# Performance work log

Measured on AMD Instinct MI355X. Metric: run time of the kernel, lower is better.

The kernel has to match this reference:

```python
import jax, jax.numpy as jnp
import numpy as np

N_NODES = 100000
N_EDGES = 1600000
IN_C, HID_C, OUT_C = 128, 64, 32


def setup_inputs() -> dict:
    key = jax.random.key(0)
    k1, k2, k3, k4 = jax.random.split(key, 4)
    x = jax.random.normal(k1, (N_NODES, IN_C), dtype=jnp.float32)
    edge_index = jax.random.randint(k2, (2, N_EDGES), 0, N_NODES, dtype=jnp.int64)
    # glorot-style init for GCN linear weights
    W1 = jax.random.normal(k3, (IN_C, HID_C), dtype=jnp.float32) * (2.0 / (IN_C + HID_C)) ** 0.5
    b1 = jnp.zeros((HID_C,), dtype=jnp.float32)
    W2 = jax.random.normal(k4, (HID_C, OUT_C), dtype=jnp.float32) * (2.0 / (HID_C + OUT_C)) ** 0.5
    b2 = jnp.zeros((OUT_C,), dtype=jnp.float32)
    return {"x": x, "edge_index": edge_index, "W1": W1, "b1": b1, "W2": W2, "b2": b2}


def _gcn_conv(h, row, col, norm, n, b):
    # gather transformed source features, scale by symmetric norm, scatter-add to targets
    msg = h[row] * norm[:, None]            # [E+N, C]
    return jax.ops.segment_sum(msg, col, num_segments=n) + b


def reference(x, edge_index, W1, b1, W2, b2):
    n = x.shape[0]
    loops = jnp.arange(n, dtype=edge_index.dtype)
    row = jnp.concatenate([edge_index[0], loops])   # sources (with self-loops)
    col = jnp.concatenate([edge_index[1], loops])   # targets
    deg = jax.ops.segment_sum(jnp.ones_like(col, dtype=x.dtype), col, num_segments=n)
    dinv = jnp.where(deg > 0, jax.lax.rsqrt(deg), 0.0)
    norm = dinv[row] * dinv[col]                    # D^{-1/2} A_hat D^{-1/2}
    h = jax.nn.relu(_gcn_conv(x @ W1, row, col, norm, n, b1))
    out = _gcn_conv(h @ W2, row, col, norm, n, b2)
    return out
```

## Files before the change

### kernel.cpp

```cpp
#include <hip/hip_runtime.h>

#define IN_C 128
#define HID_C 64
#define OUT_C 32
#define NBLK 512
#define NBUCK 512
#define CAP 5120

typedef unsigned int uint;
typedef unsigned short ushort;
typedef __attribute__((ext_vector_type(8))) short bf16x8;
typedef __attribute__((ext_vector_type(4))) float f32x4;

__device__ __forceinline__ uint bf16pair(float a, float b) {
  uint ua = __float_as_uint(a), ub = __float_as_uint(b);
  ua = (ua + 0x7FFFu + ((ua >> 16) & 1u)) >> 16;
  ub = (ub + 0x7FFFu + ((ub >> 16) & 1u)) >> 16;
  return ua | (ub << 16);
}

__device__ __forceinline__ uint bf16one(float a) {
  uint u = __float_as_uint(a);
  return (u + 0x7FFFu + ((u >> 16) & 1u)) >> 16;
}

__device__ __forceinline__ void acc8(float* acc, uint4 q) {
  acc[0] += __uint_as_float(q.x << 16);
  acc[1] += __uint_as_float(q.x & 0xFFFF0000u);
  acc[2] += __uint_as_float(q.y << 16);
  acc[3] += __uint_as_float(q.y & 0xFFFF0000u);
  acc[4] += __uint_as_float(q.z << 16);
  acc[5] += __uint_as_float(q.z & 0xFFFF0000u);
  acc[6] += __uint_as_float(q.w << 16);
  acc[7] += __uint_as_float(q.w & 0xFFFF0000u);
}


__global__ void __launch_bounds__(256) scatter_reserve_kernel(
    const int* __restrict__ row, const int* __restrict__ col,
    int* __restrict__ gcur, int* __restrict__ ebuf, int e, int epb) {
  __shared__ int hist[NBUCK];
  __shared__ int cur[NBUCK];
  int t = threadIdx.x, b = blockIdx.x;
  for (int i = t; i < NBUCK; i += 256) hist[i] = 0;
  __syncthreads();
  int s = b * epb, en = min(e, s + epb);
  for (int i = s + t; i < en; i += 256) atomicAdd(&hist[col[i] >> 8], 1);
  __syncthreads();
  for (int i = t; i < NBUCK; i += 256) {
    int h = hist[i];
    int base = h ? atomicAdd(&gcur[i], h) : 0;
    cur[i] = CAP * i + base;
  }
  __syncthreads();
  for (int i = s + t; i < en; i += 256) {
    int c = col[i], r = row[i];
    int bk = c >> 8;
    int p = atomicAdd(&cur[bk], 1);
    if (p < CAP * bk + CAP) ebuf[p] = r | ((c & 255) << 17);
  }
}

__global__ void __launch_bounds__(256) csr_kernel(const int* __restrict__ ebuf,
                                                  const int* __restrict__ gcur,
                                                  int* __restrict__ offS, int* __restrict__ offE,
                                                  int* __restrict__ srt, float* __restrict__ dinv,
                                                  int n) {
  __shared__ int cnt[256];
  __shared__ int base[256];
  int t = threadIdx.x, b = blockIdx.x;
  int es = b * CAP;
  int ec = min(gcur[b], CAP);
  cnt[t] = 0;
  __syncthreads();
  for (int i = t; i < ec; i += 256) atomicAdd(&cnt[(ebuf[es + i] >> 17) & 255], 1);
  __syncthreads();
  int v = cnt[t];
  base[t] = v;
  __syncthreads();
  for (int d = 1; d < 256; d <<= 1) {
    int a = (t >= d) ? base[t - d] : 0;
    __syncthreads();
    base[t] += a;
    __syncthreads();
  }
  int gstart = es + base[t] - v;
  int node = b * 256 + t;
  if (node < n) {
    offS[node] = gstart;
    offE[node] = gstart + v;
    dinv[node] = rsqrtf((float)(v + 1));
  }
  base[t] = gstart;
  __syncthreads();
  for (int i = t; i < ec; i += 256) {
    int pv = ebuf[es + i];
    int pos = atomicAdd(&base[(pv >> 17) & 255], 1);
    srt[pos] = pv & 0x1FFFF;
  }
}


__global__ void __launch_bounds__(256) prep_w_kernel(const float* __restrict__ W1,
                                                     const float* __restrict__ W2,
                                                     ushort* __restrict__ w1t_hi,
                                                     ushort* __restrict__ w1t_lo,
                                                     ushort* __restrict__ w2t_hi,
                                                     ushort* __restrict__ w2t_lo) {
  int t = threadIdx.x;
  for (int i = t; i < HID_C * IN_C; i += 256) {
    int c = i >> 7, k = i & 127;
    float v = W1[k * HID_C + c];
    uint h = bf16one(v);
    float lo = v - __uint_as_float(h << 16);
    w1t_hi[i] = (ushort)h;
    w1t_lo[i] = (ushort)bf16one(lo);
  }
  for (int i = t; i < OUT_C * HID_C; i += 256) {
    int c = i >> 6, k = i & 63;
    float v = W2[k * OUT_C + c];
    uint h = bf16one(v);
    float lo = v - __uint_as_float(h << 16);
    w2t_hi[i] = (ushort)h;
    w2t_lo[i] = (ushort)bf16one(lo);
  }
}

#define APAD 136
__global__ void __launch_bounds__(256) gemm1_mfma_kernel(
    const float* __restrict__ x, const ushort* __restrict__ w1t_hi,
    const ushort* __restrict__ w1t_lo, const float* __restrict__ dinv,
    ushort* __restrict__ xw1q, int n, int planeN) {
  __shared__ ushort xs_hi[64 * APAD];
  __shared__ ushort xs_lo[64 * APAD];
  __shared__ float dinv_s[64];
  int t = threadIdx.x;
  int row0 = blockIdx.x * 64;
  if (t < 64) {
    int rr = row0 + t;
    dinv_s[t] = rr < n ? dinv[rr] : 0.f;
  }
  for (int task = t; task < 64 * 16; task += 256) {
    int r = task >> 4, kc = task & 15;
    int grow = row0 + r;
    uint4 hq = {0u, 0u, 0u, 0u}, lq = {0u, 0u, 0u, 0u};
    if (grow < n) {
      const float* xp = x + (size_t)grow * IN_C + kc * 8;
      float4 v0 = *(const float4*)xp;
      float4 v1 = *(const float4*)(xp + 4);
      float vv[8] = {v0.x, v0.y, v0.z, v0.w, v1.x, v1.y, v1.z, v1.w};
      uint hu[8];
      float lf[8];
#pragma unroll
      for (int i = 0; i < 8; ++i) {
        hu[i] = bf16one(vv[i]);
        lf[i] = vv[i] - __uint_as_float(hu[i] << 16);
      }
      hq = make_uint4(hu[0] | (hu[1] << 16), hu[2] | (hu[3] << 16),
                      hu[4] | (hu[5] << 16), hu[6] | (hu[7] << 16));
      lq = make_uint4(bf16pair(lf[0], lf[1]), bf16pair(lf[2], lf[3]),
                      bf16pair(lf[4], lf[5]), bf16pair(lf[6], lf[7]));
    }
    *(uint4*)(xs_hi + r * APAD + kc * 8) = hq;
    *(uint4*)(xs_lo + r * APAD + kc * 8) = lq;
  }
  __syncthreads();
  int wv = t >> 6, lane = t & 63, m = lane & 15, q = lane >> 4;
  f32x4 acc[4];
#pragma unroll
  for (int ct = 0; ct < 4; ++ct) acc[ct] = (f32x4){0.f, 0.f, 0.f, 0.f};
  const ushort* ah_p = xs_hi + (wv * 16 + m) * APAD + q * 8;
  const ushort* al_p = xs_lo + (wv * 16 + m) * APAD + q * 8;
#pragma unroll
  for (int kb = 0; kb < 4; ++kb) {
    bf16x8 ah = *(const bf16x8*)(ah_p + kb * 32);
    bf16x8 al = *(const bf16x8*)(al_p + kb * 32);
#pragma unroll
    for (int ct = 0; ct < 4; ++ct) {
      const ushort* bp = w1t_hi + (ct * 16 + m) * IN_C + kb * 32 + q * 8;
      bf16x8 bh = *(const bf16x8*)bp;
      bf16x8 bl = *(const bf16x8*)(bp + (size_t)(w1t_lo - w1t_hi));
      acc[ct] = __builtin_amdgcn_mfma_f32_16x16x32_bf16(ah, bh, acc[ct], 0, 0, 0);
      acc[ct] = __builtin_amdgcn_mfma_f32_16x16x32_bf16(al, bh, acc[ct], 0, 0, 0);
      acc[ct] = __builtin_amdgcn_mfma_f32_16x16x32_bf16(ah, bl, acc[ct], 0, 0, 0);
    }
  }
#pragma unroll
  for (int ct = 0; ct < 4; ++ct) {
#pragma unroll
    for (int rg = 0; rg < 4; ++rg) {
      int lr = wv * 16 + q * 4 + rg;
      int grow = row0 + lr;
      if (grow < n)
        xw1q[(size_t)ct * planeN + (size_t)grow * 16 + m] =
            (ushort)bf16one(acc[ct][rg] * dinv_s[lr]);
    }
  }
}


__global__ void __launch_bounds__(256) gather1_q_kernel(
    const int* __restrict__ offS, const int* __restrict__ offE, const int* __restrict__ srt,
    const float* __restrict__ dinv, const ushort* __restrict__ xw1q,
    const float* __restrict__ b1, ushort* __restrict__ hbq, int n, int planeN) {
  int t = threadIdx.x, bid = blockIdx.x;
  int pq = bid & 3, chunk = bid >> 2;
  int g = t >> 1, fl = t & 1;
  int c = chunk * 128 + g;
  if (c >= n) return;
  const uint4* tbl = (const uint4*)(xw1q + (size_t)pq * planeN);
  int js = offS[c], je = offE[c];
  float a[8] = {0.f, 0.f, 0.f, 0.f, 0.f, 0.f, 0.f, 0.f};
  float b[8] = {0.f, 0.f, 0.f, 0.f, 0.f, 0.f, 0.f, 0.f};
  int j = js;
  for (; j + 3 < je; j += 4) {
    int r0 = __builtin_nontemporal_load(srt + j);
    int r1 = __builtin_nontemporal_load(srt + j + 1);
    int r2 = __builtin_nontemporal_load(srt + j + 2);
    int r3 = __builtin_nontemporal_load(srt + j + 3);
    uint4 q0 = tbl[(size_t)r0 * 2 + fl];
    uint4 q1 = tbl[(size_t)r1 * 2 + fl];
    uint4 q2 = tbl[(size_t)r2 * 2 + fl];
    uint4 q3 = tbl[(size_t)r3 * 2 + fl];
    acc8(a, q0); acc8(b, q1); acc8(a, q2); acc8(b, q3);
  }
  for (; j < je; ++j) {
    int r = __builtin_nontemporal_load(srt + j);
    acc8(a, tbl[(size_t)r * 2 + fl]);
  }
  acc8(a, tbl[(size_t)c * 2 + fl]);
  float dv = dinv[c];
  const float4* bv = (const float4*)b1;
  float4 b0 = bv[pq * 4 + fl * 2], b1v = bv[pq * 4 + fl * 2 + 1];
  float h0 = (a[0] + b[0]) * dv + b0.x;
  float h1 = (a[1] + b[1]) * dv + b0.y;
  float h2 = (a[2] + b[2]) * dv + b0.z;
  float h3 = (a[3] + b[3]) * dv + b0.w;
  float h4 = (a[4] + b[4]) * dv + b1v.x;
  float h5 = (a[5] + b[5]) * dv + b1v.y;
  float h6 = (a[6] + b[6]) * dv + b1v.z;
  float h7 = (a[7] + b[7]) * dv + b1v.w;
  h0 = h0 > 0.f ? h0 : 0.f; h1 = h1 > 0.f ? h1 : 0.f;
  h2 = h2 > 0.f ? h2 : 0.f; h3 = h3 > 0.f ? h3 : 0.f;
  h4 = h4 > 0.f ? h4 : 0.f; h5 = h5 > 0.f ? h5 : 0.f;
  h6 = h6 > 0.f ? h6 : 0.f; h7 = h7 > 0.f ? h7 : 0.f;
  uint4 o = make_uint4(bf16pair(h0, h1), bf16pair(h2, h3),
                       bf16pair(h4, h5), bf16pair(h6, h7));
  *(uint4*)(hbq + (size_t)pq * planeN + (size_t)c * 16 + fl * 8) = o;
}

__global__ void __launch_bounds__(256) gemm2_mfma_kernel(
    const ushort* __restrict__ hbq, const ushort* __restrict__ w2t_hi,
    const ushort* __restrict__ w2t_lo, const float* __restrict__ dinv,
    ushort* __restrict__ hw2h, int n, int planeN) {
  int t = threadIdx.x;
  int wv = t >> 6, lane = t & 63, m = lane & 15, q = lane >> 4;
  int row0 = blockIdx.x * 64 + wv * 16;
  int arow = min(row0 + m, n - 1);
  const ushort* abase = hbq + (size_t)arow * 16 + (q & 1) * 8;
  bf16x8 a0 = *(const bf16x8*)(abase + (size_t)(q >> 1) * planeN);
  bf16x8 a1 = *(const bf16x8*)(abase + (size_t)(2 + (q >> 1)) * planeN);
  f32x4 acc[2];
  acc[0] = (f32x4){0.f, 0.f, 0.f, 0.f};
  acc[1] = (f32x4){0.f, 0.f, 0.f, 0.f};
#pragma unroll
  for (int ct = 0; ct < 2; ++ct) {
    const ushort* bp = w2t_hi + (ct * 16 + m) * HID_C + q * 8;
    const ushort* blp = w2t_lo + (ct * 16 + m) * HID_C + q * 8;
    bf16x8 bh0 = *(const bf16x8*)bp;
    bf16x8 bh1 = *(const bf16x8*)(bp + 32);
    bf16x8 bl0 = *(const bf16x8*)blp;
    bf16x8 bl1 = *(const bf16x8*)(blp + 32);
    acc[ct] = __builtin_amdgcn_mfma_f32_16x16x32_bf16(a0, bh0, acc[ct], 0, 0, 0);
    acc[ct] = __builtin_amdgcn_mfma_f32_16x16x32_bf16(a1, bh1, acc[ct], 0, 0, 0);
    acc[ct] = __builtin_amdgcn_mfma_f32_16x16x32_bf16(a0, bl0, acc[ct], 0, 0, 0);
    acc[ct] = __builtin_amdgcn_mfma_f32_16x16x32_bf16(a1, bl1, acc[ct], 0, 0, 0);
  }
#pragma unroll
  for (int ct = 0; ct < 2; ++ct) {
#pragma unroll
    for (int rg = 0; rg < 4; ++rg) {
      int node = row0 + q * 4 + rg;
      if (node < n)
        hw2h[(size_t)ct * planeN + (size_t)node * 16 + m] =
            (ushort)bf16one(acc[ct][rg] * dinv[node]);
    }
  }
}

__global__ void __launch_bounds__(256) gather2_h_kernel(
    const int* __restrict__ offS, const int* __restrict__ offE, const int* __restrict__ srt,
    const float* __restrict__ dinv, const ushort* __restrict__ hw2h,
    const float* __restrict__ b2, float* __restrict__ out, int n, int planeN) {
  int t = threadIdx.x, bid = blockIdx.x;
  int ph = bid & 1, chunk = bid >> 1;
  int g = t >> 1, fl = t & 1;
  int c = chunk * 128 + g;
  if (c >= n) return;
  const uint4* tbl = (const uint4*)(hw2h + (size_t)ph * planeN);
  int js = offS[c], je = offE[c];
  float a[8] = {0.f, 0.f, 0.f, 0.f, 0.f, 0.f, 0.f, 0.f};
  float b[8] = {0.f, 0.f, 0.f, 0.f, 0.f, 0.f, 0.f, 0.f};
  int j = js;
  for (; j + 3 < je; j += 4) {
    int r0 = __builtin_nontemporal_load(srt + j);
    int r1 = __builtin_nontemporal_load(srt + j + 1);
    int r2 = __builtin_nontemporal_load(srt + j + 2);
    int r3 = __builtin_nontemporal_load(srt + j + 3);
    uint4 q0 = tbl[(size_t)r0 * 2 + fl];
    uint4 q1 = tbl[(size_t)r1 * 2 + fl];
    uint4 q2 = tbl[(size_t)r2 * 2 + fl];
    uint4 q3 = tbl[(size_t)r3 * 2 + fl];
    acc8(a, q0); acc8(b, q1); acc8(a, q2); acc8(b, q3);
  }
  for (; j < je; ++j) {
    int r = __builtin_nontemporal_load(srt + j);
    acc8(a, tbl[(size_t)r * 2 + fl]);
  }
  acc8(a, tbl[(size_t)c * 2 + fl]);
  float dv = dinv[c];
  const float4* bv = (const float4*)b2;
  float4 b0 = bv[ph * 4 + fl * 2], b1v = bv[ph * 4 + fl * 2 + 1];
  float4 olo = {(a[0] + b[0]) * dv + b0.x, (a[1] + b[1]) * dv + b0.y,
                (a[2] + b[2]) * dv + b0.z, (a[3] + b[3]) * dv + b0.w};
  float4 ohi = {(a[4] + b[4]) * dv + b1v.x, (a[5] + b[5]) * dv + b1v.y,
                (a[6] + b[6]) * dv + b1v.z, (a[7] + b[7]) * dv + b1v.w};
  float* op = out + (size_t)c * OUT_C + ph * 16 + fl * 8;
  *(float4*)op = olo;
  *(float4*)(op + 4) = ohi;
}

extern "C" void kernel_launch(void* const* d_in, const int* in_sizes, int n_in,
                              void* d_out, int out_size, void* d_ws, size_t ws_size,
                              hipStream_t stream) {
  const float* x  = (const float*)d_in[0];
  const int*   ei = (const int*)d_in[1];
  const float* W1 = (const float*)d_in[2];
  const float* b1 = (const float*)d_in[3];
  const float* W2 = (const float*)d_in[4];
  const float* b2 = (const float*)d_in[5];
  float* out = (float*)d_out;

  int n = in_sizes[0] / IN_C;
  int e = in_sizes[1] / 2;
  const int* row = ei;
  const int* col = ei + e;
  int planeN = n * 16;

  float* dinv = (float*)d_ws;
  int*   offS = (int*)(dinv + n);
  int*   offE = offS + n;
  int*   gcur = offE + n;
  int*   srt  = gcur + NBUCK;
  ushort* xw1q = (ushort*)(srt + (size_t)NBUCK * CAP);
  int*   ebuf = (int*)xw1q;
  ushort* hbq  = xw1q + (size_t)n * HID_C;
  ushort* hw2h = hbq + (size_t)n * HID_C;
  ushort* w1t_hi = hw2h + (size_t)n * OUT_C;
  ushort* w1t_lo = w1t_hi + HID_C * IN_C;
  ushort* w2t_hi = w1t_lo + HID_C * IN_C;
  ushort* w2t_lo = w2t_hi + OUT_C * HID_C;

  int epb = (e + NBLK - 1) / NBLK;
  int nbuckets = (n + 255) / 256;
  int cpp = (n + 127) / 128;

  hipMemsetAsync(gcur, 0, NBUCK * sizeof(int), stream);
  hipLaunchKernelGGL(scatter_reserve_kernel, dim3(NBLK), dim3(256), 0, stream,
                     row, col, gcur, ebuf, e, epb);
  hipLaunchKernelGGL(csr_kernel, dim3(nbuckets), dim3(256), 0, stream,
                     ebuf, gcur, offS, offE, srt, dinv, n);
  hipLaunchKernelGGL(prep_w_kernel, dim3(1), dim3(256), 0, stream,
                     W1, W2, w1t_hi, w1t_lo, w2t_hi, w2t_lo);
  hipLaunchKernelGGL(gemm1_mfma_kernel, dim3((n + 63) / 64), dim3(256), 0, stream,
                     x, w1t_hi, w1t_lo, dinv, xw1q, n, planeN);
  hipLaunchKernelGGL(gather1_q_kernel, dim3(cpp * 4), dim3(256), 0, stream,
                     offS, offE, srt, dinv, xw1q, b1, hbq, n, planeN);
  hipLaunchKernelGGL(gemm2_mfma_kernel, dim3((n + 63) / 64), dim3(256), 0, stream,
                     hbq, w2t_hi, w2t_lo, dinv, hw2h, n, planeN);
  hipLaunchKernelGGL(gather2_h_kernel, dim3(cpp * 2), dim3(256), 0, stream,
                     offS, offE, srt, dinv, hw2h, b2, out, n, planeN);
}
```

Baseline: 293.1 us.

## Partition edge gathers by source-row range for cache locality, fuse layer-1 epilogue into GEMM2

Edges within each target node are sub-sorted into four source-row quarters, and the gathers are split so that each block reads only one quarter (or half) of the feature table. The goal is to keep the random-gather working set resident in L2/MALL. Source indices shrink to 16-bit offsets, which reduces index traffic. Partial sums go out as bf16 and are combined later: layer 1's bias, ReLU and self-loop term move into the GEMM2 prologue, and a new combine kernel finishes layer 2. In exchange there are extra launches, additional bf16 rounding of partial sums, and extra partial-buffer traffic.

Measured after the change: 299.7 us. +2.3%, slower.

```diff
diff --git a/kernel.cpp b/kernel.cpp
--- a/kernel.cpp
+++ b/kernel.cpp
@@ -63,40 +63,54 @@
 
 __global__ void __launch_bounds__(256) csr_kernel(const int* __restrict__ ebuf,
                                                   const int* __restrict__ gcur,
-                                                  int* __restrict__ offS, int* __restrict__ offE,
-                                                  int* __restrict__ srt, float* __restrict__ dinv,
-                                                  int n) {
-  __shared__ int cnt[256];
-  __shared__ int base[256];
+                                                  int* __restrict__ offQ,
+                                                  ushort* __restrict__ srt,
+                                                  float* __restrict__ dinv,
+                                                  int n, int qb) {
+  __shared__ int cnt[1024];
+  __shared__ int bsum[256];
   int t = threadIdx.x, b = blockIdx.x;
   int es = b * CAP;
   int ec = min(gcur[b], CAP);
-  cnt[t] = 0;
-  __syncthreads();
-  for (int i = t; i < ec; i += 256) atomicAdd(&cnt[(ebuf[es + i] >> 17) & 255], 1);
-  __syncthreads();
-  int v = cnt[t];
-  base[t] = v;
+  for (int i = t; i < 1024; i += 256) cnt[i] = 0;
+  __syncthreads();
+  for (int i = t; i < ec; i += 256) {
+    int pv = ebuf[es + i];
+    int r = pv & 0x1FFFF;
+    int q = (r >= qb) + (r >= 2 * qb) + (r >= 3 * qb);
+    atomicAdd(&cnt[(((pv >> 17) & 255) << 2) | q], 1);
+  }
+  __syncthreads();
+  int c0 = cnt[t * 4], c1 = cnt[t * 4 + 1], c2 = cnt[t * 4 + 2], c3 = cnt[t * 4 + 3];
+  int tot = c0 + c1 + c2 + c3;
+  bsum[t] = tot;
   __syncthreads();
   for (int d = 1; d < 256; d <<= 1) {
-    int a = (t >= d) ? base[t - d] : 0;
+    int a = (t >= d) ? bsum[t - d] : 0;
     __syncthreads();
-    base[t] += a;
+    bsum[t] += a;
     __syncthreads();
   }
-  int gstart = es + base[t] - v;
+  int g0 = es + bsum[t] - tot;
+  int g1 = g0 + c0, g2 = g1 + c1, g3 = g2 + c2, g4 = g3 + c3;
   int node = b * 256 + t;
   if (node < n) {
-    offS[node] = gstart;
-    offE[node] = gstart + v;
-    dinv[node] = rsqrtf((float)(v + 1));
-  }
-  base[t] = gstart;
+    offQ[node * 5 + 0] = g0;
+    offQ[node * 5 + 1] = g1;
+    offQ[node * 5 + 2] = g2;
+    offQ[node * 5 + 3] = g3;
+    offQ[node * 5 + 4] = g4;
+    dinv[node] = rsqrtf((float)(tot + 1));
+  }
+  cnt[t * 4] = g0; cnt[t * 4 + 1] = g1; cnt[t * 4 + 2] = g2; cnt[t * 4 + 3] = g3;
   __syncthreads();
   for (int i = t; i < ec; i += 256) {
     int pv = ebuf[es + i];
-    int pos = atomicAdd(&base[(pv >> 17) & 255], 1);
-    srt[pos] = pv & 0x1FFFF;
+    int r = pv & 0x1FFFF;
+    int q = (r >= qb) + (r >= 2 * qb) + (r >= 3 * qb);
+    int key = (((pv >> 17) & 255) << 2) | q;
+    int pos = atomicAdd(&cnt[key], 1);
+    srt[pos] = (ushort)(r - (q >> 1) * (2 * qb));
   }
 }
 
@@ -127,10 +141,11 @@
 }
 
 #define APAD 136
+#define EPAD 68
 __global__ void __launch_bounds__(256) gemm1_mfma_kernel(
     const float* __restrict__ x, const ushort* __restrict__ w1t_hi,
     const ushort* __restrict__ w1t_lo, const float* __restrict__ dinv,
-    ushort* __restrict__ xw1q, int n, int planeN) {
+    ushort* __restrict__ xw1b, int n) {
   __shared__ ushort xs_hi[64 * APAD];
   __shared__ ushort xs_lo[64 * APAD];
   __shared__ float dinv_s[64];
@@ -185,81 +200,96 @@
       acc[ct] = __builtin_amdgcn_mfma_f32_16x16x32_bf16(ah, bl, acc[ct], 0, 0, 0);
     }
   }
-#pragma unroll
-  for (int ct = 0; ct < 4; ++ct) {
-#pragma unroll
-    for (int rg = 0; rg < 4; ++rg) {
-      int lr = wv * 16 + q * 4 + rg;
-      int grow = row0 + lr;
-      if (grow < n)
-        xw1q[(size_t)ct * planeN + (size_t)grow * 16 + m] =
-            (ushort)bf16one(acc[ct][rg] * dinv_s[lr]);
+  __syncthreads();
+  float* eps = (float*)xs_hi;
+#pragma unroll
+  for (int ct = 0; ct < 4; ++ct)
+#pragma unroll
+    for (int rg = 0; rg < 4; ++rg)
+      eps[(wv * 16 + q * 4 + rg) * EPAD + ct * 16 + m] = acc[ct][rg];
+  __syncthreads();
+  for (int task = t; task < 64 * 16; task += 256) {
+    int r = task >> 4, cc = task & 15;
+    int grow = row0 + r;
+    if (grow < n) {
+      float4 v = *(const float4*)&eps[r * EPAD + cc * 4];
+      float dv = dinv_s[r];
+      uint2 o = make_uint2(bf16pair(v.x * dv, v.y * dv), bf16pair(v.z * dv, v.w * dv));
+      ((uint2*)(xw1b + (size_t)grow * HID_C))[cc] = o;
     }
   }
 }
 
-
 __global__ void __launch_bounds__(256) gather1_q_kernel(
-    const int* __restrict__ offS, const int* __restrict__ offE, const int* __restrict__ srt,
-    const float* __restrict__ dinv, const ushort* __restrict__ xw1q,
-    const float* __restrict__ b1, ushort* __restrict__ hbq, int n, int planeN) {
+    const int* __restrict__ offQ, const ushort* __restrict__ srt,
+    const ushort* __restrict__ xw1b, ushort* __restrict__ pacc1,
+    int base, int rowEnd, int prows, int qb) {
   int t = threadIdx.x, bid = blockIdx.x;
-  int pq = bid & 3, chunk = bid >> 2;
-  int g = t >> 1, fl = t & 1;
-  int c = chunk * 128 + g;
-  if (c >= n) return;
-  const uint4* tbl = (const uint4*)(xw1q + (size_t)pq * planeN);
-  int js = offS[c], je = offE[c];
+  int q = bid & 3, fh = (bid >> 2) & 1, chunk = bid >> 3;
+  int g = t >> 2, fl = t & 3;
+  int c = base + chunk * 64 + g;
+  if (c >= rowEnd) return;
+  int js = offQ[c * 5 + q], je = offQ[c * 5 + q + 1];
+  int rbase = (q >> 1) * (2 * qb);
+  const uint4* tbl = (const uint4*)xw1b;
+  int sel = fh * 4 + fl;
   float a[8] = {0.f, 0.f, 0.f, 0.f, 0.f, 0.f, 0.f, 0.f};
   float b[8] = {0.f, 0.f, 0.f, 0.f, 0.f, 0.f, 0.f, 0.f};
   int j = js;
   for (; j + 3 < je; j += 4) {
-    int r0 = __builtin_nontemporal_load(srt + j);
-    int r1 = __builtin_nontemporal_load(srt + j + 1);
-    int r2 = __builtin_nontemporal_load(srt + j + 2);
-    int r3 = __builtin_nontemporal_load(srt + j + 3);
-    uint4 q0 = tbl[(size_t)r0 * 2 + fl];
-    uint4 q1 = tbl[(size_t)r1 * 2 + fl];
-    uint4 q2 = tbl[(size_t)r2 * 2 + fl];
-    uint4 q3 = tbl[(size_t)r3 * 2 + fl];
-    acc8(a, q0); acc8(b, q1); acc8(a, q2); acc8(b, q3);
+    int r0 = (int)__builtin_nontemporal_load(srt + j) + rbase;
+    int r1 = (int)__builtin_nontemporal_load(srt + j + 1) + rbase;
+    int r2 = (int)__builtin_nontemporal_load(srt + j + 2) + rbase;
+    int r3 = (int)__builtin_nontemporal_load(srt + j + 3) + rbase;
+    acc8(a, tbl[(size_t)r0 * 8 + sel]);
+    acc8(b, tbl[(size_t)r1 * 8 + sel]);
+    acc8(a, tbl[(size_t)r2 * 8 + sel]);
+    acc8(b, tbl[(size_t)r3 * 8 + sel]);
   }
   for (; j < je; ++j) {
-    int r = __builtin_nontemporal_load(srt + j);
-    acc8(a, tbl[(size_t)r * 2 + fl]);
-  }
-  acc8(a, tbl[(size_t)c * 2 + fl]);
-  float dv = dinv[c];
-  const float4* bv = (const float4*)b1;
-  float4 b0 = bv[pq * 4 + fl * 2], b1v = bv[pq * 4 + fl * 2 + 1];
-  float h0 = (a[0] + b[0]) * dv + b0.x;
-  float h1 = (a[1] + b[1]) * dv + b0.y;
-  float h2 = (a[2] + b[2]) * dv + b0.z;
-  float h3 = (a[3] + b[3]) * dv + b0.w;
-  float h4 = (a[4] + b[4]) * dv + b1v.x;
-  float h5 = (a[5] + b[5]) * dv + b1v.y;
-  float h6 = (a[6] + b[6]) * dv + b1v.z;
-  float h7 = (a[7] + b[7]) * dv + b1v.w;
-  h0 = h0 > 0.f ? h0 : 0.f; h1 = h1 > 0.f ? h1 : 0.f;
-  h2 = h2 > 0.f ? h2 : 0.f; h3 = h3 > 0.f ? h3 : 0.f;
-  h4 = h4 > 0.f ? h4 : 0.f; h5 = h5 > 0.f ? h5 : 0.f;
-  h6 = h6 > 0.f ? h6 : 0.f; h7 = h7 > 0.f ? h7 : 0.f;
-  uint4 o = make_uint4(bf16pair(h0, h1), bf16pair(h2, h3),
-                       bf16pair(h4, h5), bf16pair(h6, h7));
-  *(uint4*)(hbq + (size_t)pq * planeN + (size_t)c * 16 + fl * 8) = o;
-}
-
+    int r = (int)__builtin_nontemporal_load(srt + j) + rbase;
+    acc8(a, tbl[(size_t)r * 8 + sel]);
+  }
+  uint4 o = make_uint4(bf16pair(a[0] + b[0], a[1] + b[1]),
+                       bf16pair(a[2] + b[2], a[3] + b[3]),
+                       bf16pair(a[4] + b[4], a[5] + b[5]),
+                       bf16pair(a[6] + b[6], a[7] + b[7]));
+  *(uint4*)(pacc1 + ((size_t)(q * 2 + fh) * prows + (c - base)) * 32 + fl * 8) = o;
+}
+
+#define EPAD2 36
 __global__ void __launch_bounds__(256) gemm2_mfma_kernel(
-    const ushort* __restrict__ hbq, const ushort* __restrict__ w2t_hi,
+    const ushort* __restrict__ pacc1, const ushort* __restrict__ xw1b,
+    const float* __restrict__ b1, const ushort* __restrict__ w2t_hi,
     const ushort* __restrict__ w2t_lo, const float* __restrict__ dinv,
-    ushort* __restrict__ hw2h, int n, int planeN) {
+    ushort* __restrict__ hw2b, int base, int rowEnd, int prows) {
+  __shared__ float eps[64 * EPAD2];
   int t = threadIdx.x;
   int wv = t >> 6, lane = t & 63, m = lane & 15, q = lane >> 4;
-  int row0 = blockIdx.x * 64 + wv * 16;
-  int arow = min(row0 + m, n - 1);
-  const ushort* abase = hbq + (size_t)arow * 16 + (q & 1) * 8;
-  bf16x8 a0 = *(const bf16x8*)(abase + (size_t)(q >> 1) * planeN);
-  bf16x8 a1 = *(const bf16x8*)(abase + (size_t)(2 + (q >> 1)) * planeN);
+  int rblk = base + blockIdx.x * 64;
+  int arow = min(rblk + wv * 16 + m, rowEnd - 1);
+  float dv_a = dinv[arow];
+  bf16x8 afr[2];
+#pragma unroll
+  for (int part = 0; part < 2; ++part) {
+    float s[8] = {0.f, 0.f, 0.f, 0.f, 0.f, 0.f, 0.f, 0.f};
+    acc8(s, ((const uint4*)xw1b)[(size_t)arow * 8 + part * 4 + q]);
+#pragma unroll
+    for (int qq = 0; qq < 4; ++qq)
+      acc8(s, ((const uint4*)pacc1)[((size_t)(qq * 2 + part) * prows + (arow - base)) * 4 + q]);
+    float4 bb0 = ((const float4*)b1)[part * 8 + q * 2];
+    float4 bb1 = ((const float4*)b1)[part * 8 + q * 2 + 1];
+    float h[8];
+    h[0] = s[0] * dv_a + bb0.x; h[1] = s[1] * dv_a + bb0.y;
+    h[2] = s[2] * dv_a + bb0.z; h[3] = s[3] * dv_a + bb0.w;
+    h[4] = s[4] * dv_a + bb1.x; h[5] = s[5] * dv_a + bb1.y;
+    h[6] = s[6] * dv_a + bb1.z; h[7] = s[7] * dv_a + bb1.w;
+#pragma unroll
+    for (int i = 0; i < 8; ++i) h[i] = h[i] > 0.f ? h[i] : 0.f;
+    uint4 u = make_uint4(bf16pair(h[0], h[1]), bf16pair(h[2], h[3]),
+                         bf16pair(h[4], h[5]), bf16pair(h[6], h[7]));
+    afr[part] = *(bf16x8*)&u;
+  }
   f32x4 acc[2];
   acc[0] = (f32x4){0.f, 0.f, 0.f, 0.f};
   acc[1] = (f32x4){0.f, 0.f, 0.f, 0.f};
@@ -271,63 +301,82 @@
     bf16x8 bh1 = *(const bf16x8*)(bp + 32);
     bf16x8 bl0 = *(const bf16x8*)blp;
     bf16x8 bl1 = *(const bf16x8*)(blp + 32);
-    acc[ct] = __builtin_amdgcn_mfma_f32_16x16x32_bf16(a0, bh0, acc[ct], 0, 0, 0);
-    acc[ct] = __builtin_amdgcn_mfma_f32_16x16x32_bf16(a1, bh1, acc[ct], 0, 0, 0);
-    acc[ct] = __builtin_amdgcn_mfma_f32_16x16x32_bf16(a0, bl0, acc[ct], 0, 0, 0);
-    acc[ct] = __builtin_amdgcn_mfma_f32_16x16x32_bf16(a1, bl1, acc[ct], 0, 0, 0);
-  }
-#pragma unroll
-  for (int ct = 0; ct < 2; ++ct) {
-#pragma unroll
-    for (int rg = 0; rg < 4; ++rg) {
-      int node = row0 + q * 4 + rg;
-      if (node < n)
-        hw2h[(size_t)ct * planeN + (size_t)node * 16 + m] =
-            (ushort)bf16one(acc[ct][rg] * dinv[node]);
+    acc[ct] = __builtin_amdgcn_mfma_f32_16x16x32_bf16(afr[0], bh0, acc[ct], 0, 0, 0);
+    acc[ct] = __builtin_amdgcn_mfma_f32_16x16x32_bf16(afr[1], bh1, acc[ct], 0, 0, 0);
+    acc[ct] = __builtin_amdgcn_mfma_f32_16x16x32_bf16(afr[0], bl0, acc[ct], 0, 0, 0);
+    acc[ct] = __builtin_amdgcn_mfma_f32_16x16x32_bf16(afr[1], bl1, acc[ct], 0, 0, 0);
+  }
+#pragma unroll
+  for (int ct = 0; ct < 2; ++ct)
+#pragma unroll
+    for (int rg = 0; rg < 4; ++rg)
+      eps[(wv * 16 + q * 4 + rg) * EPAD2 + ct * 16 + m] = acc[ct][rg];
+  __syncthreads();
+  for (int task = t; task < 64 * 8; task += 256) {
+    int r = task >> 3, cc = task & 7;
+    int node = rblk + r;
+    if (node < rowEnd) {
+      float4 v = *(const float4*)&eps[r * EPAD2 + cc * 4];
+      float dv = dinv[node];
+      uint2 o = make_uint2(bf16pair(v.x * dv, v.y * dv), bf16pair(v.z * dv, v.w * dv));
+      ((uint2*)(hw2b + (size_t)node * OUT_C))[cc] = o;
     }
   }
 }
 
 __global__ void __launch_bounds__(256) gather2_h_kernel(
-    const int* __restrict__ offS, const int* __restrict__ offE, const int* __restrict__ srt,
-    const float* __restrict__ dinv, const ushort* __restrict__ hw2h,
-    const float* __restrict__ b2, float* __restrict__ out, int n, int planeN) {
+    const int* __restrict__ offQ, const ushort* __restrict__ srt,
+    const ushort* __restrict__ hw2b, ushort* __restrict__ pacc2, int n, int qb) {
   int t = threadIdx.x, bid = blockIdx.x;
-  int ph = bid & 1, chunk = bid >> 1;
-  int g = t >> 1, fl = t & 1;
-  int c = chunk * 128 + g;
+  int q2 = bid & 1, chunk = bid >> 1;
+  int g = t >> 2, fl = t & 3;
+  int c = chunk * 64 + g;
   if (c >= n) return;
-  const uint4* tbl = (const uint4*)(hw2h + (size_t)ph * planeN);
-  int js = offS[c], je = offE[c];
+  int js = offQ[c * 5 + 2 * q2], je = offQ[c * 5 + 2 * q2 + 2];
+  int rbase = q2 * 2 * qb;
+  const uint4* tbl = (const uint4*)hw2b;
   float a[8] = {0.f, 0.f, 0.f, 0.f, 0.f, 0.f, 0.f, 0.f};
   float b[8] = {0.f, 0.f, 0.f, 0.f, 0.f, 0.f, 0.f, 0.f};
   int j = js;
   for (; j + 3 < je; j += 4) {
-    int r0 = __builtin_nontemporal_load(srt + j);
-    int r1 = __builtin_nontemporal_load(srt + j + 1);
-    int r2 = __builtin_nontemporal_load(srt + j + 2);
-    int r3 = __builtin_nontemporal_load(srt + j + 3);
-    uint4 q0 = tbl[(size_t)r0 * 2 + fl];
-    uint4 q1 = tbl[(size_t)r1 * 2 + fl];
-    uint4 q2 = tbl[(size_t)r2 * 2 + fl];
-    uint4 q3 = tbl[(size_t)r3 * 2 + fl];
-    acc8(a, q0); acc8(b, q1); acc8(a, q2); acc8(b, q3);
+    int r0 = (int)__builtin_nontemporal_load(srt + j) + rbase;
+    int r1 = (int)__builtin_nontemporal_load(srt + j + 1) + rbase;
+    int r2 = (int)__builtin_nontemporal_load(srt + j + 2) + rbase;
+    int r3 = (int)__builtin_nontemporal_load(srt + j + 3) + rbase;
+    acc8(a, tbl[(size_t)r0 * 4 + fl]);
+    acc8(b, tbl[(size_t)r1 * 4 + fl]);
+    acc8(a, tbl[(size_t)r2 * 4 + fl]);
+    acc8(b, tbl[(size_t)r3 * 4 + fl]);
   }
   for (; j < je; ++j) {
-    int r = __builtin_nontemporal_load(srt + j);
-    acc8(a, tbl[(size_t)r * 2 + fl]);
-  }
-  acc8(a, tbl[(size_t)c * 2 + fl]);
+    int r = (int)__builtin_nontemporal_load(srt + j) + rbase;
+    acc8(a, tbl[(size_t)r * 4 + fl]);
+  }
+  uint4 o = make_uint4(bf16pair(a[0] + b[0], a[1] + b[1]),
+                       bf16pair(a[2] + b[2], a[3] + b[3]),
+                       bf16pair(a[4] + b[4], a[5] + b[5]),
+                       bf16pair(a[6] + b[6], a[7] + b[7]));
+  *(uint4*)(pacc2 + ((size_t)q2 * n + c) * 32 + fl * 8) = o;
+}
+
+__global__ void __launch_bounds__(256) combine2_kernel(
+    const ushort* __restrict__ pacc2, const ushort* __restrict__ hw2b,
+    const float* __restrict__ dinv, const float* __restrict__ b2,
+    float* __restrict__ out, int n) {
+  int idx = blockIdx.x * 256 + threadIdx.x;
+  if (idx >= n * 16) return;
+  int c = idx >> 4, d = idx & 15;
+  uint p0 = ((const uint*)pacc2)[(size_t)c * 16 + d];
+  uint p1 = ((const uint*)pacc2)[((size_t)n + c) * 16 + d];
+  uint sf = ((const uint*)hw2b)[(size_t)c * 16 + d];
   float dv = dinv[c];
-  const float4* bv = (const float4*)b2;
-  float4 b0 = bv[ph * 4 + fl * 2], b1v = bv[ph * 4 + fl * 2 + 1];
-  float4 olo = {(a[0] + b[0]) * dv + b0.x, (a[1] + b[1]) * dv + b0.y,
-                (a[2] + b[2]) * dv + b0.z, (a[3] + b[3]) * dv + b0.w};
-  float4 ohi = {(a[4] + b[4]) * dv + b1v.x, (a[5] + b[5]) * dv + b1v.y,
-                (a[6] + b[6]) * dv + b1v.z, (a[7] + b[7]) * dv + b1v.w};
-  float* op = out + (size_t)c * OUT_C + ph * 16 + fl * 8;
-  *(float4*)op = olo;
-  *(float4*)(op + 4) = ohi;
+  float2 bb = ((const float2*)b2)[d];
+  float2 o;
+  o.x = (__uint_as_float(p0 << 16) + __uint_as_float(p1 << 16) +
+         __uint_as_float(sf << 16)) * dv + bb.x;
+  o.y = (__uint_as_float(p0 & 0xFFFF0000u) + __uint_as_float(p1 & 0xFFFF0000u) +
+         __uint_as_float(sf & 0xFFFF0000u)) * dv + bb.y;
+  ((float2*)out)[idx] = o;
 }
 
 extern "C" void kernel_launch(void* const* d_in, const int* in_sizes, int n_in,
@@ -345,39 +394,47 @@
   int e = in_sizes[1] / 2;
   const int* row = ei;
   const int* col = ei + e;
-  int planeN = n * 16;
-
-  float* dinv = (float*)d_ws;
-  int*   offS = (int*)(dinv + n);
-  int*   offE = offS + n;
-  int*   gcur = offE + n;
-  int*   srt  = gcur + NBUCK;
-  ushort* xw1q = (ushort*)(srt + (size_t)NBUCK * CAP);
-  int*   ebuf = (int*)xw1q;
-  ushort* hbq  = xw1q + (size_t)n * HID_C;
-  ushort* hw2h = hbq + (size_t)n * HID_C;
-  ushort* w1t_hi = hw2h + (size_t)n * OUT_C;
+  int qb = (n + 3) / 4;
+  int half = n / 2;
+
+  float*  dinv  = (float*)d_ws;
+  int*    offQ  = (int*)(dinv + n);
+  int*    gcur  = offQ + (size_t)n * 5;
+  ushort* srt   = (ushort*)(gcur + NBUCK);
+  ushort* xw1b  = srt + (size_t)NBUCK * CAP;
+  ushort* pacc1 = xw1b + (size_t)n * HID_C;
+  int*    ebuf  = (int*)pacc1;
+  ushort* hw2b  = pacc1 + (size_t)8 * half * 32;
+  ushort* pacc2 = xw1b;
+  ushort* w1t_hi = hw2b + (size_t)n * OUT_C;
   ushort* w1t_lo = w1t_hi + HID_C * IN_C;
   ushort* w2t_hi = w1t_lo + HID_C * IN_C;
   ushort* w2t_lo = w2t_hi + OUT_C * HID_C;
 
   int epb = (e + NBLK - 1) / NBLK;
   int nbuckets = (n + 255) / 256;
-  int cpp = (n + 127) / 128;
+  int ch1 = (half + 63) / 64;
+  int ch2 = (n + 63) / 64;
 
   hipMemsetAsync(gcur, 0, NBUCK * sizeof(int), stream);
   hipLaunchKernelGGL(scatter_reserve_kernel, dim3(NBLK), dim3(256), 0, stream,
                      row, col, gcur, ebuf, e, epb);
   hipLaunchKernelGGL(csr_kernel, dim3(nbuckets), dim3(256), 0, stream,
-                     ebuf, gcur, offS, offE, srt, dinv, n);
+                     ebuf, gcur, offQ, srt, dinv, n, qb);
   hipLaunchKernelGGL(prep_w_kernel, dim3(1), dim3(256), 0, stream,
                      W1, W2, w1t_hi, w1t_lo, w2t_hi, w2t_lo);
   hipLaunchKernelGGL(gemm1_mfma_kernel, dim3((n + 63) / 64), dim3(256), 0, stream,
-                     x, w1t_hi, w1t_lo, dinv, xw1q, n, planeN);
-  hipLaunchKernelGGL(gather1_q_kernel, dim3(cpp * 4), dim3(256), 0, stream,
-                     offS, offE, srt, dinv, xw1q, b1, hbq, n, planeN);
-  hipLaunchKernelGGL(gemm2_mfma_kernel, dim3((n + 63) / 64), dim3(256), 0, stream,
-                     hbq, w2t_hi, w2t_lo, dinv, hw2h, n, planeN);
-  hipLaunchKernelGGL(gather2_h_kernel, dim3(cpp * 2), dim3(256), 0, stream,
-                     offS, offE, srt, dinv, hw2h, b2, out, n, planeN);
-}
+                     x, w1t_hi, w1t_lo, dinv, xw1b, n);
+  hipLaunchKernelGGL(gather1_q_kernel, dim3(ch1 * 8), dim3(256), 0, stream,
+                     offQ, srt, xw1b, pacc1, 0, half, half, qb);
+  hipLaunchKernelGGL(gemm2_mfma_kernel, dim3(ch1), dim3(256), 0, stream,
+                     pacc1, xw1b, b1, w2t_hi, w2t_lo, dinv, hw2b, 0, half, half);
+  hipLaunchKernelGGL(gather1_q_kernel, dim3(ch1 * 8), dim3(256), 0, stream,
+                     offQ, srt, xw1b, pacc1, half, n, half, qb);
+  hipLaunchKernelGGL(gemm2_mfma_kernel, dim3(ch1), dim3(256), 0, stream,
+                     pacc1, xw1b, b1, w2t_hi, w2t_lo, dinv, hw2b, half, n, half);
+  hipLaunchKernelGGL(gather2_h_kernel, dim3(ch2 * 2), dim3(256), 0, stream,
+                     offQ, srt, hw2b, pacc2, n, qb);
+  hipLaunchKernelGGL(combine2_kernel, dim3((n * 16 + 255) / 256), dim3(256), 0, stream,
+                     pacc2, hw2b, dinv, b2, out, n);
+}
```
